# Kernel tuning notes

Hardware: AMD Instinct MI355X
Metric: run time of the kernel (lower is better)

## Reference

```python
import jax, jax.numpy as jnp
import numpy as np

EPS = 1e-7  # SimplifiedLayerNorm eps


def setup_inputs() -> dict:
    key = jax.random.key(0)
    k1, k2 = jax.random.split(key)
    x = jax.random.normal(k1, (8, 2048, 64), dtype=jnp.float32)   # [B, T, d]
    W = jax.random.normal(k2, (2048, 8), dtype=jnp.float32)       # [T, H] per-distance, per-head Toeplitz weights
    return {"x": x, "W": W}


def _l2norm(v):
    return v / (jnp.linalg.norm(v, axis=-1, keepdims=True) + EPS)


def reference(x, W):
    B, T, d = x.shape
    H = W.shape[1]
    # pad one zero token: [B, T+1, d]
    xp = jnp.concatenate([x, jnp.zeros((B, 1, d), x.dtype)], axis=1)
    idx = jnp.arange(T + 1)
    dist = idx[:, None] - idx[None, :]                 # [T+1, T+1], row - col
    # Toeplitz logits: W[dist, h] for 0 <= dist < T; the single dist==T entry
    # (bottom-left corner) is left at its initial 0.0; dist < 0 is causally masked.
    Wd = W[jnp.clip(dist, 0, T - 1)]                   # [T+1, T+1, H]
    dist3 = dist[..., None]
    logits = jnp.where(dist3 < 0, -jnp.inf,
                       jnp.where(dist3 >= T, jnp.zeros((), x.dtype), Wd))
    probs = jax.nn.softmax(logits, axis=1)             # softmax over columns (dim=-1 of W_h)
    v = jnp.einsum('tsh,bsd->hbtd', probs, xp)         # [H, B, T+1, d]
    v = _l2norm(v)
    V = jnp.concatenate([v, xp[None]], axis=0)         # [H+1, B, T+1, d]
    V = _l2norm(V)
    return V
```

## Files before the change

### kernel.cpp

```cpp
#include <hip/hip_runtime.h>

#define EPS 1e-7f
#define T_DIM 2048
#define TP1   2049
#define H_DIM 8
#define B_DIM 8
#define SP    2080
#define NFRAG 138
#define FB_OFF 32
#define RSTRIDE 66

typedef short v8s __attribute__((ext_vector_type(8)));
typedef float v4f __attribute__((ext_vector_type(4)));

static __device__ __forceinline__ unsigned short f2bf(float f) {
  union { float f; unsigned u; } v; v.f = f;
  unsigned r = v.u + 0x7fffu + ((v.u >> 16) & 1u);
  return (unsigned short)(r >> 16);
}

#define J1_BLOCKS 276
#define J2_BLOCKS 264
#define J3_BLOCKS 4098

__global__ __launch_bounds__(256) void prep(const float* __restrict__ x,
                                            const float* __restrict__ W,
                                            unsigned short* __restrict__ fragA,
                                            unsigned short* __restrict__ xT,
                                            float* __restrict__ out) {
  __shared__ float tile[64][65];
  int bid = blockIdx.x;
  if (bid < J1_BLOCKS) {
    int tid = bid * 256 + threadIdx.x;
    int blk = tid >> 6, lane = tid & 63;
    int h = blk / NFRAG, fb = blk - h * NFRAG;
    int b0 = fb * 16 - FB_OFF;
    int lm = lane & 15, quad = lane >> 4;
    v8s frag;
    #pragma unroll
    for (int j = 0; j < 8; ++j) {
      int d = b0 + lm - 8 * quad - j;
      float v = 0.0f;
      if (d >= 0 && d < T_DIM) v = __expf(W[d * H_DIM + h]);
      else if (d == T_DIM) v = 1.0f;
      frag[j] = (short)f2bf(v);
    }
    *(v8s*)(fragA + (size_t)tid * 8) = frag;
    return;
  }
  bid -= J1_BLOCKS;
  if (bid < J2_BLOCKS) {
    int b = bid / 33, st = bid % 33;
    int tid = threadIdx.x;
    if (st == 32) {
      #pragma unroll
      for (int i = 0; i < 8; ++i) {
        int idx = tid * 8 + i;
        int dd = idx >> 5, sl = idx & 31;
        xT[((size_t)b * 64 + dd) * SP + T_DIM + sl] = 0;
      }
      return;
    }
    int s0 = st * 64;
    int c = tid & 63, r4 = tid >> 6;
    #pragma unroll
    for (int i = 0; i < 16; ++i) {
      int sl = r4 * 16 + i;
      tile[sl][c] = x[((size_t)b * T_DIM + (s0 + sl)) * 64 + c];
    }
    __syncthreads();
    #pragma unroll
    for (int i = 0; i < 16; ++i) {
      int dd = r4 * 16 + i;
      xT[((size_t)b * 64 + dd) * SP + s0 + c] = f2bf(tile[c][dd]);
    }
    return;
  }
  bid -= J2_BLOCKS;
  {
    int row = bid * 4 + (threadIdx.x >> 6);
    if (row >= B_DIM * TP1) return;
    int b = row / TP1, t = row - b * TP1;
    int dd = threadIdx.x & 63;
    float v = (t < T_DIM) ? x[((size_t)b * T_DIM + t) * 64 + dd] : 0.0f;
    float ss = v * v;
    ss += __shfl_xor(ss, 1);  ss += __shfl_xor(ss, 2);
    ss += __shfl_xor(ss, 4);  ss += __shfl_xor(ss, 8);
    ss += __shfl_xor(ss, 16); ss += __shfl_xor(ss, 32);
    float inv = 1.0f / (sqrtf(ss) + EPS);
    __builtin_nontemporal_store(v * inv,
        &out[(((size_t)(H_DIM * B_DIM + b) * TP1 + t) << 6) + dd]);
  }
}

__global__ __launch_bounds__(256) void toeplitz_mm(const unsigned short* __restrict__ fragA,
                                                   const unsigned short* __restrict__ xT,
                                                   float* __restrict__ out) {
  __shared__ float red[2][64 * RSTRIDE];

  const int lane = threadIdx.x & 63;
  const int w    = threadIdx.x >> 6;
  const int wm   = w & 1;
  const int wk   = w >> 1;
  const int lm   = lane & 15;
  const int quad = lane >> 4;

  const int bi  = blockIdx.x;
  const int tb  = 16 - (bi >> 6);
  const int rem = bi & 63;
  const int h = rem & 7, b = (rem >> 3) & 7;
  const int t0 = tb * 128;
  const int tw = t0 + 64 * wm;

  const unsigned short* fA = fragA + ((size_t)h * NFRAG * 64 + lane) * 8;
  const unsigned short* xb = xT + ((size_t)b * 64 + lm) * SP + 8 * quad;

  const int sw_end = min(tw + 32, T_DIM);

  v4f acc[4][4] = {};

  v8s a0[4], a1[4], b0[4], b1[4];

#define LOAD_A(dst, s0v) do {                                        \
    const v8s* _p = (const v8s*)(fA + (size_t)((tw - (s0v) + FB_OFF) >> 4) * 512); \
    dst[0] = _p[0]; dst[1] = _p[64]; dst[2] = _p[128]; dst[3] = _p[192]; } while (0)
#define LOAD_B(dst, s0v) do {                                        \
    const unsigned short* _p = xb + (s0v);                           \
    dst[0] = *(const v8s*)(_p);                                      \
    dst[1] = *(const v8s*)(_p + 16 * SP);                            \
    dst[2] = *(const v8s*)(_p + 32 * SP);                            \
    dst[3] = *(const v8s*)(_p + 48 * SP); } while (0)
#define DO_MFMA(fa, fb) do {                                         \
    _Pragma("unroll")                                                \
    for (int mt = 0; mt < 4; ++mt)                                   \
      _Pragma("unroll")                                              \
      for (int nt = 0; nt < 4; ++nt)                                 \
        acc[mt][nt] = __builtin_amdgcn_mfma_f32_16x16x32_bf16(fa[mt], fb[nt], acc[mt][nt], 0, 0, 0); } while (0)

  int s0 = 32 * wk;
  LOAD_A(a0, s0); LOAD_B(b0, s0);
  for (;;) {
    bool more = (s0 + 64 <= sw_end);
    if (more) { LOAD_A(a1, s0 + 64); LOAD_B(b1, s0 + 64); }
    DO_MFMA(a0, b0);
    if (!more) break;
    s0 += 64;
    bool more2 = (s0 + 64 <= sw_end);
    if (more2) { LOAD_A(a0, s0 + 64); LOAD_B(b0, s0 + 64); }
    DO_MFMA(a1, b1);
    if (!more2) break;
    s0 += 64;
  }

  if (wk == 1) {
    float* buf = red[wm];
    #pragma unroll
    for (int mt = 0; mt < 4; ++mt)
      #pragma unroll
      for (int r = 0; r < 4; ++r) {
        int row = 16 * mt + 4 * quad + r;
        #pragma unroll
        for (int nt = 0; nt < 4; ++nt)
          buf[row * RSTRIDE + 16 * nt + lm] = acc[mt][nt][r];
      }
  }
  __syncthreads();
  if (wk != 0) return;

  const float* buf = red[wm];
  #pragma unroll
  for (int mt = 0; mt < 4; ++mt) {
    #pragma unroll
    for (int r = 0; r < 4; ++r) {
      int row = 16 * mt + 4 * quad + r;
      #pragma unroll
      for (int nt = 0; nt < 4; ++nt)
        acc[mt][nt][r] += buf[row * RSTRIDE + 16 * nt + lm];
    }
  }

  #pragma unroll
  for (int mt = 0; mt < 4; ++mt) {
    #pragma unroll
    for (int r = 0; r < 4; ++r) {
      float ss = 0.0f;
      #pragma unroll
      for (int nt = 0; nt < 4; ++nt) { float a = acc[mt][nt][r]; ss += a * a; }
      ss += __shfl_xor(ss, 1);
      ss += __shfl_xor(ss, 2);
      ss += __shfl_xor(ss, 4);
      ss += __shfl_xor(ss, 8);
      int t = tw + 16 * mt + 4 * quad + r;
      if (t <= T_DIM) {
        float n1 = sqrtf(ss);
        float u  = n1 / (n1 + EPS);
        float inv = 1.0f / ((n1 + EPS) * (u + EPS));
        float* op = out + (((size_t)(h * B_DIM + b) * TP1 + t) << 6) + lm;
        #pragma unroll
        for (int nt = 0; nt < 4; ++nt)
          __builtin_nontemporal_store(acc[mt][nt][r] * inv, op + 16 * nt);
      }
    }
  }
}

extern "C" void kernel_launch(void* const* d_in, const int* in_sizes, int n_in,
                              void* d_out, int out_size, void* d_ws, size_t ws_size,
                              hipStream_t stream) {
  const float* x = (const float*)d_in[0];
  const float* W = (const float*)d_in[1];
  float* out = (float*)d_out;

  unsigned short* xT    = (unsigned short*)d_ws;
  unsigned short* fragA = (unsigned short*)((char*)d_ws + 2131968);

  hipLaunchKernelGGL(prep, dim3(J1_BLOCKS + J2_BLOCKS + J3_BLOCKS), dim3(256), 0, stream,
                     x, W, fragA, xT, out);
  hipLaunchKernelGGL(toeplitz_mm, dim3(64 * 17), dim3(256), 0, stream, fragA, xT, out);
}
```

Measured before the change: 115.1 us.

## Rebalance Toeplitz matmul into per-wave paired strip jobs, move last row to prep

The matmul kernel's block decomposition is replaced. Previously each block had two row halves with split-K across waves and an LDS reduction. Now each wave owns a 32-row strip with the full K range and processes two jobs, a long strip paired with a short one, so work is balanced across 512 blocks. The special last row (t=T) moves into the prep kernel as a scalar fp32 dot-product job. This removes the LDS reduction and the barrier. In exchange each wave carries a longer serial K loop and there is less MFMA-level parallelism per block.

```diff
diff --git a/kernel.cpp b/kernel.cpp
--- a/kernel.cpp
+++ b/kernel.cpp
@@ -8,7 +8,7 @@
 #define SP    2080
 #define NFRAG 138
 #define FB_OFF 32
-#define RSTRIDE 66
+#define NJOBS 4096
 
 typedef short v8s __attribute__((ext_vector_type(8)));
 typedef float v4f __attribute__((ext_vector_type(4)));
@@ -22,6 +22,7 @@
 #define J1_BLOCKS 276
 #define J2_BLOCKS 264
 #define J3_BLOCKS 4098
+#define J4_BLOCKS 64
 
 __global__ __launch_bounds__(256) void prep(const float* __restrict__ x,
                                             const float* __restrict__ W,
@@ -29,6 +30,7 @@
                                             unsigned short* __restrict__ xT,
                                             float* __restrict__ out) {
   __shared__ float tile[64][65];
+  __shared__ float red4[4][64];
   int bid = blockIdx.x;
   if (bid < J1_BLOCKS) {
     int tid = bid * 256 + threadIdx.x;
@@ -77,7 +79,7 @@
     return;
   }
   bid -= J2_BLOCKS;
-  {
+  if (bid < J3_BLOCKS) {
     int row = bid * 4 + (threadIdx.x >> 6);
     if (row >= B_DIM * TP1) return;
     int b = row / TP1, t = row - b * TP1;
@@ -90,40 +92,63 @@
     float inv = 1.0f / (sqrtf(ss) + EPS);
     __builtin_nontemporal_store(v * inv,
         &out[(((size_t)(H_DIM * B_DIM + b) * TP1 + t) << 6) + dd]);
+    return;
+  }
+  bid -= J3_BLOCKS;
+  {
+    int h = bid >> 3, b = bid & 7;
+    int dd = threadIdx.x & 63, c = threadIdx.x >> 6;
+    float a = 0.0f;
+    #pragma unroll 4
+    for (int i = 0; i < 512; ++i) {
+      int s = c * 512 + i;
+      float k = (s == 0) ? 1.0f : __expf(W[(T_DIM - s) * H_DIM + h]);
+      a = fmaf(k, x[((size_t)b * T_DIM + s) * 64 + dd], a);
+    }
+    red4[c][dd] = a;
+    __syncthreads();
+    if (threadIdx.x < 64) {
+      float v = red4[0][dd] + red4[1][dd] + red4[2][dd] + red4[3][dd];
+      float ss = v * v;
+      ss += __shfl_xor(ss, 1);  ss += __shfl_xor(ss, 2);
+      ss += __shfl_xor(ss, 4);  ss += __shfl_xor(ss, 8);
+      ss += __shfl_xor(ss, 16); ss += __shfl_xor(ss, 32);
+      float n1 = sqrtf(ss);
+      float u  = n1 / (n1 + EPS);
+      float inv = 1.0f / ((n1 + EPS) * (u + EPS));
+      __builtin_nontemporal_store(v * inv,
+          &out[(((size_t)(h * B_DIM + b) * TP1 + T_DIM) << 6) + dd]);
+    }
   }
 }
 
 __global__ __launch_bounds__(256) void toeplitz_mm(const unsigned short* __restrict__ fragA,
                                                    const unsigned short* __restrict__ xT,
                                                    float* __restrict__ out) {
-  __shared__ float red[2][64 * RSTRIDE];
-
   const int lane = threadIdx.x & 63;
   const int w    = threadIdx.x >> 6;
-  const int wm   = w & 1;
-  const int wk   = w >> 1;
   const int lm   = lane & 15;
   const int quad = lane >> 4;
-
-  const int bi  = blockIdx.x;
-  const int tb  = 16 - (bi >> 6);
-  const int rem = bi & 63;
-  const int h = rem & 7, b = (rem >> 3) & 7;
-  const int t0 = tb * 128;
-  const int tw = t0 + 64 * wm;
-
-  const unsigned short* fA = fragA + ((size_t)h * NFRAG * 64 + lane) * 8;
-  const unsigned short* xb = xT + ((size_t)b * 64 + lm) * SP + 8 * quad;
-
-  const int sw_end = min(tw + 32, T_DIM);
-
-  v4f acc[4][4] = {};
-
-  v8s a0[4], a1[4], b0[4], b1[4];
-
-#define LOAD_A(dst, s0v) do {                                        \
-    const v8s* _p = (const v8s*)(fA + (size_t)((tw - (s0v) + FB_OFF) >> 4) * 512); \
-    dst[0] = _p[0]; dst[1] = _p[64]; dst[2] = _p[128]; dst[3] = _p[192]; } while (0)
+  const int gid  = blockIdx.x * 4 + w;
+
+  #pragma unroll 1
+  for (int job = 0; job < 2; ++job) {
+    const int jj    = job ? (NJOBS - 1 - gid) : gid;
+    const int strip = 63 - (jj >> 6);
+    const int combo = jj & 63;
+    const int h = combo & 7, b = combo >> 3;
+    const int tw = strip * 32;
+
+    const unsigned short* fA = fragA + ((size_t)h * NFRAG * 64 + lane) * 8;
+    const unsigned short* xb = xT + ((size_t)b * 64 + lm) * SP + 8 * quad;
+    const int s_last = tw;
+
+    v4f acc[2][4] = {};
+    v8s a0[2], a1[2], b0[4], b1[4];
+
+#define LOAD_A(dst, s0v) do {                                                        \
+    dst[0] = *(const v8s*)(fA + (size_t)((tw      - (s0v) + FB_OFF) >> 4) * 512);    \
+    dst[1] = *(const v8s*)(fA + (size_t)((tw + 16 - (s0v) + FB_OFF) >> 4) * 512); } while (0)
 #define LOAD_B(dst, s0v) do {                                        \
     const unsigned short* _p = xb + (s0v);                           \
     dst[0] = *(const v8s*)(_p);                                      \
@@ -132,66 +157,38 @@
     dst[3] = *(const v8s*)(_p + 48 * SP); } while (0)
 #define DO_MFMA(fa, fb) do {                                         \
     _Pragma("unroll")                                                \
-    for (int mt = 0; mt < 4; ++mt)                                   \
+    for (int mt = 0; mt < 2; ++mt)                                   \
       _Pragma("unroll")                                              \
       for (int nt = 0; nt < 4; ++nt)                                 \
         acc[mt][nt] = __builtin_amdgcn_mfma_f32_16x16x32_bf16(fa[mt], fb[nt], acc[mt][nt], 0, 0, 0); } while (0)
 
-  int s0 = 32 * wk;
-  LOAD_A(a0, s0); LOAD_B(b0, s0);
-  for (;;) {
-    bool more = (s0 + 64 <= sw_end);
-    if (more) { LOAD_A(a1, s0 + 64); LOAD_B(b1, s0 + 64); }
-    DO_MFMA(a0, b0);
-    if (!more) break;
-    s0 += 64;
-    bool more2 = (s0 + 64 <= sw_end);
-    if (more2) { LOAD_A(a0, s0 + 64); LOAD_B(b0, s0 + 64); }
-    DO_MFMA(a1, b1);
-    if (!more2) break;
-    s0 += 64;
-  }
-
-  if (wk == 1) {
-    float* buf = red[wm];
-    #pragma unroll
-    for (int mt = 0; mt < 4; ++mt)
+    int s0 = 0;
+    LOAD_A(a0, 0); LOAD_B(b0, 0);
+    for (;;) {
+      bool more = (s0 + 32 <= s_last);
+      if (more) { LOAD_A(a1, s0 + 32); LOAD_B(b1, s0 + 32); }
+      DO_MFMA(a0, b0);
+      if (!more) break;
+      s0 += 32;
+      bool more2 = (s0 + 32 <= s_last);
+      if (more2) { LOAD_A(a0, s0 + 32); LOAD_B(b0, s0 + 32); }
+      DO_MFMA(a1, b1);
+      if (!more2) break;
+      s0 += 32;
+    }
+
+    #pragma unroll
+    for (int mt = 0; mt < 2; ++mt) {
       #pragma unroll
       for (int r = 0; r < 4; ++r) {
-        int row = 16 * mt + 4 * quad + r;
+        float ss = 0.0f;
         #pragma unroll
-        for (int nt = 0; nt < 4; ++nt)
-          buf[row * RSTRIDE + 16 * nt + lm] = acc[mt][nt][r];
-      }
-  }
-  __syncthreads();
-  if (wk != 0) return;
-
-  const float* buf = red[wm];
-  #pragma unroll
-  for (int mt = 0; mt < 4; ++mt) {
-    #pragma unroll
-    for (int r = 0; r < 4; ++r) {
-      int row = 16 * mt + 4 * quad + r;
-      #pragma unroll
-      for (int nt = 0; nt < 4; ++nt)
-        acc[mt][nt][r] += buf[row * RSTRIDE + 16 * nt + lm];
-    }
-  }
-
-  #pragma unroll
-  for (int mt = 0; mt < 4; ++mt) {
-    #pragma unroll
-    for (int r = 0; r < 4; ++r) {
-      float ss = 0.0f;
-      #pragma unroll
-      for (int nt = 0; nt < 4; ++nt) { float a = acc[mt][nt][r]; ss += a * a; }
-      ss += __shfl_xor(ss, 1);
-      ss += __shfl_xor(ss, 2);
-      ss += __shfl_xor(ss, 4);
-      ss += __shfl_xor(ss, 8);
-      int t = tw + 16 * mt + 4 * quad + r;
-      if (t <= T_DIM) {
+        for (int nt = 0; nt < 4; ++nt) { float a = acc[mt][nt][r]; ss += a * a; }
+        ss += __shfl_xor(ss, 1);
+        ss += __shfl_xor(ss, 2);
+        ss += __shfl_xor(ss, 4);
+        ss += __shfl_xor(ss, 8);
+        int t = tw + 16 * mt + 4 * quad + r;
         float n1 = sqrtf(ss);
         float u  = n1 / (n1 + EPS);
         float inv = 1.0f / ((n1 + EPS) * (u + EPS));
@@ -202,6 +199,9 @@
       }
     }
   }
+#undef LOAD_A
+#undef LOAD_B
+#undef DO_MFMA
 }
 
 extern "C" void kernel_launch(void* const* d_in, const int* in_sizes, int n_in,
@@ -214,7 +214,7 @@
   unsigned short* xT    = (unsigned short*)d_ws;
   unsigned short* fragA = (unsigned short*)((char*)d_ws + 2131968);
 
-  hipLaunchKernelGGL(prep, dim3(J1_BLOCKS + J2_BLOCKS + J3_BLOCKS), dim3(256), 0, stream,
-                     x, W, fragA, xT, out);
-  hipLaunchKernelGGL(toeplitz_mm, dim3(64 * 17), dim3(256), 0, stream, fragA, xT, out);
-}
+  hipLaunchKernelGGL(prep, dim3(J1_BLOCKS + J2_BLOCKS + J3_BLOCKS + J4_BLOCKS), dim3(256),
+                     0, stream, x, W, fragA, xT, out);
+  hipLaunchKernelGGL(toeplitz_mm, dim3(128 * 4), dim3(256), 0, stream, fragA, xT, out);
+}
```

After: 165.7 us. 1.44x slower.

## Give each wave its own 64-row strip and reuse A fragments across K steps

Applied to the files above, without the earlier changes.

The Toeplitz matmul kernel now assigns one independent 64-row output strip per wave, so the split-K LDS reduction and block barrier go away. A register ring of eight A fragments exploits the Toeplitz structure so that each 32-column K step loads only two new fragments instead of four, with a three-deep B prefetch. A rank permutation spreads long and short strips across blocks. The normalized passthrough of x is also fused into the transpose stage of the prep kernel, which removes the separate row-norm blocks and a second read of x. In exchange each wave runs a longer serial K loop with less parallelism per strip, and the register pressure is higher.

```diff
diff --git a/kernel.cpp b/kernel.cpp
--- a/kernel.cpp
+++ b/kernel.cpp
@@ -8,7 +8,6 @@
 #define SP    2080
 #define NFRAG 138
 #define FB_OFF 32
-#define RSTRIDE 66
 
 typedef short v8s __attribute__((ext_vector_type(8)));
 typedef float v4f __attribute__((ext_vector_type(4)));
@@ -21,7 +20,6 @@
 
 #define J1_BLOCKS 276
 #define J2_BLOCKS 264
-#define J3_BLOCKS 4098
 
 __global__ __launch_bounds__(256) void prep(const float* __restrict__ x,
                                             const float* __restrict__ W,
@@ -49,7 +47,7 @@
     return;
   }
   bid -= J1_BLOCKS;
-  if (bid < J2_BLOCKS) {
+  {
     int b = bid / 33, st = bid % 33;
     int tid = threadIdx.x;
     if (st == 32) {
@@ -59,6 +57,11 @@
         int dd = idx >> 5, sl = idx & 31;
         xT[((size_t)b * 64 + dd) * SP + T_DIM + sl] = 0;
       }
+      if (b == 0) {
+        for (int i = tid; i < 512; i += 256)
+          __builtin_nontemporal_store(0.0f,
+            &out[(((size_t)(H_DIM * B_DIM + (i >> 6)) * TP1 + T_DIM) << 6) + (i & 63)]);
+      }
       return;
     }
     int s0 = st * 64;
@@ -74,110 +77,87 @@
       int dd = r4 * 16 + i;
       xT[((size_t)b * 64 + dd) * SP + s0 + c] = f2bf(tile[c][dd]);
     }
-    return;
-  }
-  bid -= J2_BLOCKS;
-  {
-    int row = bid * 4 + (threadIdx.x >> 6);
-    if (row >= B_DIM * TP1) return;
-    int b = row / TP1, t = row - b * TP1;
-    int dd = threadIdx.x & 63;
-    float v = (t < T_DIM) ? x[((size_t)b * T_DIM + t) * 64 + dd] : 0.0f;
-    float ss = v * v;
-    ss += __shfl_xor(ss, 1);  ss += __shfl_xor(ss, 2);
-    ss += __shfl_xor(ss, 4);  ss += __shfl_xor(ss, 8);
-    ss += __shfl_xor(ss, 16); ss += __shfl_xor(ss, 32);
-    float inv = 1.0f / (sqrtf(ss) + EPS);
-    __builtin_nontemporal_store(v * inv,
-        &out[(((size_t)(H_DIM * B_DIM + b) * TP1 + t) << 6) + dd]);
+    #pragma unroll
+    for (int i = 0; i < 16; ++i) {
+      int row = r4 * 16 + i;
+      float v = tile[row][c];
+      float ss = v * v;
+      ss += __shfl_xor(ss, 1);  ss += __shfl_xor(ss, 2);
+      ss += __shfl_xor(ss, 4);  ss += __shfl_xor(ss, 8);
+      ss += __shfl_xor(ss, 16); ss += __shfl_xor(ss, 32);
+      float inv = 1.0f / (sqrtf(ss) + EPS);
+      __builtin_nontemporal_store(v * inv,
+          &out[(((size_t)(H_DIM * B_DIM + b) * TP1 + (s0 + row)) << 6) + c]);
+    }
   }
 }
 
 __global__ __launch_bounds__(256) void toeplitz_mm(const unsigned short* __restrict__ fragA,
                                                    const unsigned short* __restrict__ xT,
                                                    float* __restrict__ out) {
-  __shared__ float red[2][64 * RSTRIDE];
-
   const int lane = threadIdx.x & 63;
   const int w    = threadIdx.x >> 6;
-  const int wm   = w & 1;
-  const int wk   = w >> 1;
   const int lm   = lane & 15;
   const int quad = lane >> 4;
 
-  const int bi  = blockIdx.x;
-  const int tb  = 16 - (bi >> 6);
-  const int rem = bi & 63;
-  const int h = rem & 7, b = (rem >> 3) & 7;
-  const int t0 = tb * 128;
-  const int tw = t0 + 64 * wm;
+  const int bi   = blockIdx.x;
+  const int rank = (bi < 256) ? bi : (bi < 512 ? 767 - bi : bi);
+  const int j    = rank * 4 + w;
+  const int strip = 32 - (j >> 6);
+  const int combo = j & 63;
+  const int h = combo & 7, b = combo >> 3;
+  const int tw = strip * 64;
 
   const unsigned short* fA = fragA + ((size_t)h * NFRAG * 64 + lane) * 8;
   const unsigned short* xb = xT + ((size_t)b * 64 + lm) * SP + 8 * quad;
-
-  const int sw_end = min(tw + 32, T_DIM);
+  const int s_last = min(tw + 32, T_DIM);
+  const int fbase  = (tw + FB_OFF) >> 4;
 
   v4f acc[4][4] = {};
-
-  v8s a0[4], a1[4], b0[4], b1[4];
-
-#define LOAD_A(dst, s0v) do {                                        \
-    const v8s* _p = (const v8s*)(fA + (size_t)((tw - (s0v) + FB_OFF) >> 4) * 512); \
-    dst[0] = _p[0]; dst[1] = _p[64]; dst[2] = _p[128]; dst[3] = _p[192]; } while (0)
-#define LOAD_B(dst, s0v) do {                                        \
-    const unsigned short* _p = xb + (s0v);                           \
+  v8s As[8];
+  v8s Bs[4][4];
+
+#define SLOT(mt, P) (((mt) + 16 - 2 * (P)) & 7)
+#define LOAD_B(dst, sv) do {                                         \
+    const unsigned short* _p = xb + (sv);                            \
     dst[0] = *(const v8s*)(_p);                                      \
     dst[1] = *(const v8s*)(_p + 16 * SP);                            \
     dst[2] = *(const v8s*)(_p + 32 * SP);                            \
     dst[3] = *(const v8s*)(_p + 48 * SP); } while (0)
-#define DO_MFMA(fa, fb) do {                                         \
-    _Pragma("unroll")                                                \
-    for (int mt = 0; mt < 4; ++mt)                                   \
-      _Pragma("unroll")                                              \
-      for (int nt = 0; nt < 4; ++nt)                                 \
-        acc[mt][nt] = __builtin_amdgcn_mfma_f32_16x16x32_bf16(fa[mt], fb[nt], acc[mt][nt], 0, 0, 0); } while (0)
-
-  int s0 = 32 * wk;
-  LOAD_A(a0, s0); LOAD_B(b0, s0);
-  for (;;) {
-    bool more = (s0 + 64 <= sw_end);
-    if (more) { LOAD_A(a1, s0 + 64); LOAD_B(b1, s0 + 64); }
-    DO_MFMA(a0, b0);
-    if (!more) break;
-    s0 += 64;
-    bool more2 = (s0 + 64 <= sw_end);
-    if (more2) { LOAD_A(a0, s0 + 64); LOAD_B(b0, s0 + 64); }
-    DO_MFMA(a1, b1);
-    if (!more2) break;
-    s0 += 64;
-  }
-
-  if (wk == 1) {
-    float* buf = red[wm];
-    #pragma unroll
-    for (int mt = 0; mt < 4; ++mt)
-      #pragma unroll
-      for (int r = 0; r < 4; ++r) {
-        int row = 16 * mt + 4 * quad + r;
-        #pragma unroll
-        for (int nt = 0; nt < 4; ++nt)
-          buf[row * RSTRIDE + 16 * nt + lm] = acc[mt][nt][r];
-      }
-  }
-  __syncthreads();
-  if (wk != 0) return;
-
-  const float* buf = red[wm];
+
   #pragma unroll
-  for (int mt = 0; mt < 4; ++mt) {
-    #pragma unroll
-    for (int r = 0; r < 4; ++r) {
-      int row = 16 * mt + 4 * quad + r;
-      #pragma unroll
-      for (int nt = 0; nt < 4; ++nt)
-        acc[mt][nt][r] += buf[row * RSTRIDE + 16 * nt + lm];
-    }
-  }
+  for (int k = 0; k < 8; ++k) {
+    int fb = fbase + ((k + 4) & 7) - 4;
+    if (fb < 0) fb = 0;
+    As[k] = *(const v8s*)(fA + (size_t)fb * 512);
+  }
+  LOAD_B(Bs[0], 0);
+  { int s1 = min(32, s_last); LOAD_B(Bs[1], s1); }
+  { int s2 = min(64, s_last); LOAD_B(Bs[2], s2); }
+
+  int s0 = 0;
+
+#define PHASE(P) {                                                            \
+    { const v8s* _bq = Bs[(P) & 3];                                           \
+      _Pragma("unroll")                                                       \
+      for (int nt = 0; nt < 4; ++nt) {                                        \
+        acc[0][nt] = __builtin_amdgcn_mfma_f32_16x16x32_bf16(As[SLOT(0,P)], _bq[nt], acc[0][nt], 0, 0, 0); \
+        acc[1][nt] = __builtin_amdgcn_mfma_f32_16x16x32_bf16(As[SLOT(1,P)], _bq[nt], acc[1][nt], 0, 0, 0); \
+        acc[2][nt] = __builtin_amdgcn_mfma_f32_16x16x32_bf16(As[SLOT(2,P)], _bq[nt], acc[2][nt], 0, 0, 0); \
+        acc[3][nt] = __builtin_amdgcn_mfma_f32_16x16x32_bf16(As[SLOT(3,P)], _bq[nt], acc[3][nt], 0, 0, 0); \
+      } }                                                                     \
+    if (s0 == s_last) goto done;                                              \
+    { int _fb = (tw - s0 - 64) >> 4;                        \
+      int _f0 = _fb > 0 ? _fb : 0;                                            \
+      int _f1 = (_fb + 1) > 0 ? (_fb + 1) : 0;                                \
+      As[SLOT(0, (P) + 3)] = *(const v8s*)(fA + (size_t)_f0 * 512);           \
+      As[SLOT(1, (P) + 3)] = *(const v8s*)(fA + (size_t)_f1 * 512);           \
+      int _sp = s0 + 96; if (_sp > s_last) _sp = s_last;                      \
+      LOAD_B(Bs[((P) + 3) & 3], _sp); }                                       \
+    s0 += 32; }
+
+  for (;;) { PHASE(0) PHASE(1) PHASE(2) PHASE(3) }
+done:
 
   #pragma unroll
   for (int mt = 0; mt < 4; ++mt) {
@@ -202,6 +182,9 @@
       }
     }
   }
+#undef PHASE
+#undef LOAD_B
+#undef SLOT
 }
 
 extern "C" void kernel_launch(void* const* d_in, const int* in_sizes, int n_in,
@@ -214,7 +197,7 @@
   unsigned short* xT    = (unsigned short*)d_ws;
   unsigned short* fragA = (unsigned short*)((char*)d_ws + 2131968);
 
-  hipLaunchKernelGGL(prep, dim3(J1_BLOCKS + J2_BLOCKS + J3_BLOCKS), dim3(256), 0, stream,
+  hipLaunchKernelGGL(prep, dim3(J1_BLOCKS + J2_BLOCKS), dim3(256), 0, stream,
                      x, W, fragA, xT, out);
-  hipLaunchKernelGGL(toeplitz_mm, dim3(64 * 17), dim3(256), 0, stream, fragA, xT, out);
-}
+  hipLaunchKernelGGL(toeplitz_mm, dim3(528), dim3(256), 0, stream, fragA, xT, out);
+}
```

Measured after the change: 115.7 us. No clear change (+0.5%).
